# Optimization experiments

Measured on AMD Instinct MI355X. Metric: run time of the kernel, lower is better.

Reference implementation:

```python
import math
import jax, jax.numpy as jnp
import numpy as np

S = 2048
D_MOD = 1024
D_K = 64
D_V = 64
H = 16
MASKED = True


def setup_inputs() -> dict:
    key = jax.random.key(0)
    ks = jax.random.split(key, 11)
    sc_in = 1.0 / math.sqrt(D_MOD)
    sc_o = 1.0 / math.sqrt(H * D_V)
    return {
        "Q_input": jax.random.normal(ks[0], (S, D_MOD), jnp.float32),
        "K_input": jax.random.normal(ks[1], (S, D_MOD), jnp.float32),
        "V_input": jax.random.normal(ks[2], (S, D_MOD), jnp.float32),
        # stacked per-head Linear params (torch Linear: y = x @ W.T + b)
        "WQw": jax.random.uniform(ks[3], (H, D_K, D_MOD), jnp.float32, -sc_in, sc_in),
        "WQb": jax.random.uniform(ks[4], (H, D_K), jnp.float32, -sc_in, sc_in),
        "WKw": jax.random.uniform(ks[5], (H, D_K, D_MOD), jnp.float32, -sc_in, sc_in),
        "WKb": jax.random.uniform(ks[6], (H, D_K), jnp.float32, -sc_in, sc_in),
        "WVw": jax.random.uniform(ks[7], (H, D_V, D_MOD), jnp.float32, -sc_in, sc_in),
        "WVb": jax.random.uniform(ks[8], (H, D_V), jnp.float32, -sc_in, sc_in),
        "WOw": jax.random.uniform(ks[9], (D_MOD, H * D_V), jnp.float32, -sc_o, sc_o),
        "WOb": jax.random.uniform(ks[10], (D_MOD,), jnp.float32, -sc_o, sc_o),
    }


def reference(Q_input, K_input, V_input, WQw, WQb, WKw, WKb, WVw, WVb, WOw, WOb):
    # per-head projections, batched over heads: [H, S, d]
    q = jnp.einsum("sd,hkd->hsk", Q_input, WQw) + WQb[:, None, :]
    k = jnp.einsum("sd,hkd->hsk", K_input, WKw) + WKb[:, None, :]
    v = jnp.einsum("sd,hvd->hsv", V_input, WVw) + WVb[:, None, :]
    # raw scores [H, S, T]
    qk = jnp.einsum("hsk,htk->hst", q, k)
    if MASKED:
        qk = jnp.tril(qk)  # torch.tril: zero (not -inf) upper triangle
    # torch log_softmax(dim=0) on each [S, T] matrix -> axis 1 of [H, S, T]
    scores = jax.nn.log_softmax(qk / math.sqrt(D_K), axis=1)
    attn = jnp.einsum("hst,htv->hsv", scores, v)  # [H, S, d_v]
    # torch.cat(head_attns, dim=1) -> [S, H*d_v], head-major feature order
    Z = jnp.transpose(attn, (1, 0, 2)).reshape(S, H * D_V)
    return Z @ WOw.T + WOb
```

## Files before the change

### kernel.cpp

```cpp
#include <hip/hip_runtime.h>
#include <math.h>
#include <stdint.h>

#define S 2048
#define DMOD 1024
#define H 16

typedef unsigned short ushort_t;
typedef short bf16x8 __attribute__((ext_vector_type(8)));
typedef float f32x4 __attribute__((ext_vector_type(4)));

#define SW(r) ((((r) & 7)) ^ ((((r) >> 3) & 3) << 1))

__device__ __forceinline__ ushort_t f2b(float f) {
    union { float f; unsigned u; } x; x.f = f;
    return (ushort_t)((x.u + 0x7FFFu + ((x.u >> 16) & 1u)) >> 16);
}
__device__ __forceinline__ float b2f(ushort_t b) {
    union { unsigned u; float f; } x; x.u = ((unsigned)b) << 16;
    return x.f;
}
__device__ __forceinline__ void gld16(const ushort_t* g, ushort_t* l) {
    __builtin_amdgcn_global_load_lds(
        (const __attribute__((address_space(1))) unsigned int*)g,
        (__attribute__((address_space(3))) unsigned int*)l, 16, 0, 0);
}

__global__ __launch_bounds__(256) void init_all(
    float* __restrict__ attn_raw, float* __restrict__ out,
    float* __restrict__ sumexp, float* __restrict__ corr)
{
    const int b = blockIdx.x;
    const float4 z4 = {0.f, 0.f, 0.f, 0.f};
    if (b < 2048) {
        *(float4*)(attn_raw + ((size_t)b * 256 + threadIdx.x) * 4) = z4;
    } else if (b < 4096) {
        *(float4*)(out + ((size_t)(b - 2048) * 256 + threadIdx.x) * 4) = z4;
    } else if (b < 4128) {
        int e = ((b - 4096) * 256 + threadIdx.x) * 4;
        float4 v = {(float)(e & 2047), (float)((e + 1) & 2047),
                    (float)((e + 2) & 2047), (float)((e + 3) & 2047)};
        *(float4*)(sumexp + e) = v;
    } else {
        *(float4*)(corr + threadIdx.x * 4) = z4;
    }
}

__global__ __launch_bounds__(256) void convert_all(
    const float* q, const float* k, const float* v,
    const float* wq, const float* wk, const float* wv, const float* wo,
    ushort_t* qo, ushort_t* ko, ushort_t* vo,
    ushort_t* wqo, ushort_t* wko, ushort_t* wvo, ushort_t* woo)
{
    const int seg = blockIdx.y;
    const float* src; ushort_t* dst; size_t off = 0;
    const size_t M1 = (size_t)1 << 20;
    if (seg < 2)       { src = q;  dst = qo;  off = (size_t)seg * M1; }
    else if (seg < 4)  { src = k;  dst = ko;  off = (size_t)(seg - 2) * M1; }
    else if (seg < 6)  { src = v;  dst = vo;  off = (size_t)(seg - 4) * M1; }
    else if (seg == 6) { src = wq; dst = wqo; }
    else if (seg == 7) { src = wk; dst = wko; }
    else if (seg == 8) { src = wv; dst = wvo; }
    else               { src = wo; dst = woo; }
    size_t i = off + ((size_t)blockIdx.x * 256 + threadIdx.x) * 4;
    float4 f = *(const float4*)(src + i);
    union { uint2 u2; ushort_t us[4]; } o;
    o.us[0] = f2b(f.x); o.us[1] = f2b(f.y); o.us[2] = f2b(f.z); o.us[3] = f2b(f.w);
    *(uint2*)(dst + i) = o.u2;
}

__global__ __launch_bounds__(256) void gemm_qkv(
    const ushort_t* __restrict__ A0, const ushort_t* __restrict__ A1,
    const ushort_t* __restrict__ A2, const ushort_t* __restrict__ Wqkv,
    const float* __restrict__ b0, const float* __restrict__ b1,
    const float* __restrict__ b2,
    ushort_t* __restrict__ qbb, ushort_t* __restrict__ kbb,
    ushort_t* __restrict__ vt)
{
    __shared__ ushort_t As[128 * 64];
    __shared__ ushort_t Bs[64 * 64];
    const int tid = threadIdx.x;
    const int lane = tid & 63, wid = tid >> 6;
    const int quad = lane >> 4, l15 = lane & 15;
    const int wr = wid >> 1, wc = wid & 1;
    const int m0 = blockIdx.y * 128;
    const int n0 = blockIdx.x * 64;
    const int seg = n0 >> 10;
    const int nloc = n0 & 1023;
    const ushort_t* A = seg == 0 ? A0 : (seg == 1 ? A1 : A2);
    const float* bias = seg == 0 ? b0 : (seg == 1 ? b1 : b2);

    const f32x4 fz = {0.f, 0.f, 0.f, 0.f};
    f32x4 acc[4][2];
#pragma unroll
    for (int i = 0; i < 4; ++i) { acc[i][0] = fz; acc[i][1] = fz; }

    for (int k0 = 0; k0 < DMOD; k0 += 64) {
        __syncthreads();
#pragma unroll
        for (int i = 0; i < 4; ++i) {
            int c = i * 256 + tid, row = c >> 3, kcl = c & 7;
            gld16(A + (size_t)(m0 + row) * DMOD + k0 + (kcl ^ SW(row)) * 8, &As[c * 8]);
        }
#pragma unroll
        for (int i = 0; i < 2; ++i) {
            int c = i * 256 + tid, row = c >> 3, kcl = c & 7;
            gld16(Wqkv + (size_t)(n0 + row) * DMOD + k0 + (kcl ^ SW(row)) * 8, &Bs[c * 8]);
        }
        __syncthreads();
#pragma unroll
        for (int kc = 0; kc < 2; ++kc) {
            bf16x8 af[4], bfr[2];
#pragma unroll
            for (int mi = 0; mi < 4; ++mi) {
                int row = wr * 64 + mi * 16 + l15;
                af[mi] = *(const bf16x8*)&As[row * 64 + ((kc * 4 + quad) ^ SW(row)) * 8];
            }
#pragma unroll
            for (int ni = 0; ni < 2; ++ni) {
                int row = wc * 32 + ni * 16 + l15;
                bfr[ni] = *(const bf16x8*)&Bs[row * 64 + ((kc * 4 + quad) ^ SW(row)) * 8];
            }
#pragma unroll
            for (int mi = 0; mi < 4; ++mi)
#pragma unroll
                for (int ni = 0; ni < 2; ++ni)
                    acc[mi][ni] = __builtin_amdgcn_mfma_f32_16x16x32_bf16(
                        af[mi], bfr[ni], acc[mi][ni], 0, 0, 0);
        }
    }

    if (seg < 2) {
        ushort_t* C = seg == 0 ? qbb : kbb;
#pragma unroll
        for (int mi = 0; mi < 4; ++mi)
#pragma unroll
            for (int ni = 0; ni < 2; ++ni) {
                int gn = nloc + wc * 32 + ni * 16 + l15;
                float bv = bias[gn];
#pragma unroll
                for (int r = 0; r < 4; ++r) {
                    int gm = m0 + wr * 64 + mi * 16 + quad * 4 + r;
                    C[(size_t)gm * DMOD + gn] = f2b(acc[mi][ni][r] + bv);
                }
            }
    } else {
#pragma unroll
        for (int mi = 0; mi < 4; ++mi)
#pragma unroll
            for (int ni = 0; ni < 2; ++ni) {
                int gn = nloc + wc * 32 + ni * 16 + l15;
                float bv = bias[gn];
                int gmb = m0 + wr * 64 + mi * 16 + quad * 4;
                union { uint2 u2; ushort_t us[4]; } o;
#pragma unroll
                for (int r = 0; r < 4; ++r) o.us[r] = f2b(acc[mi][ni][r] + bv);
                *(uint2*)&vt[(size_t)gn * S + gmb] = o.u2;
            }
    }
}

__global__ __launch_bounds__(512, 4) void attn_mfma(
    const ushort_t* __restrict__ qb, const ushort_t* __restrict__ kb,
    const ushort_t* __restrict__ vt, float* __restrict__ attn_raw,
    float* __restrict__ sumexp)
{
    __shared__ ushort_t Qs[128 * 64];
    __shared__ ushort_t Ks[2][4096];
    __shared__ ushort_t Vs[2][4096];
    __shared__ ushort_t Ps[128 * 64];
    __shared__ float    sacc[1024];

    const int h = blockIdx.y;
    const int bx = blockIdx.x;
    const int si = 15 - (bx >> 1);
    const int z = bx & 1;
    const int half = si + 1;
    const int tbeg = z ? half : 0;
    const int tend = z ? 2 * si + 2 : half;
    const int s0 = si * 128;

    const int tid = threadIdx.x;
    const int lane = tid & 63, w = tid >> 6;
    const int quad = lane >> 4, l15 = lane & 15;
    const int sband = s0 + w * 16;

    const ushort_t* qh = qb + h * 64;
    const ushort_t* kh = kb + h * 64;
    const ushort_t* vh = vt + (size_t)(h * 64) * S;

#pragma unroll
    for (int i = 0; i < 2; ++i) {
        int c = i * 512 + tid, row = c >> 3, kcl = c & 7;
        gld16(qh + (size_t)(s0 + row) * DMOD + (kcl ^ SW(row)) * 8, &Qs[c * 8]);
    }
    {
        int t0 = tbeg * 64;
        int row = tid >> 3, kcl = tid & 7;
        gld16(kh + (size_t)(t0 + row) * DMOD + (kcl ^ SW(row)) * 8, &Ks[0][tid * 8]);
        gld16(vh + (size_t)row * S + t0 + (kcl ^ SW(row)) * 8, &Vs[0][tid * 8]);
    }
    for (int i = tid; i < 1024; i += 512) sacc[i] = 0.f;
    __syncthreads();

    bf16x8 aq[2];
    {
        int rq = w * 16 + l15;
#pragma unroll
        for (int kc = 0; kc < 2; ++kc)
            aq[kc] = *(const bf16x8*)&Qs[rq * 64 + ((kc * 4 + quad) ^ SW(rq)) * 8];
    }

    const f32x4 fz = {0.f, 0.f, 0.f, 0.f};
    f32x4 oacc[4];
#pragma unroll
    for (int ni = 0; ni < 4; ++ni) oacc[ni] = fz;

    for (int it = tbeg; it < tend; ++it) {
        const int p = (it - tbeg) & 1;
        const int t0 = it * 64;
        if (it + 1 < tend) {
            int t1 = t0 + 64;
            int row = tid >> 3, kcl = tid & 7;
            gld16(kh + (size_t)(t1 + row) * DMOD + (kcl ^ SW(row)) * 8, &Ks[1 - p][tid * 8]);
            gld16(vh + (size_t)row * S + t1 + (kcl ^ SW(row)) * 8, &Vs[1 - p][tid * 8]);
        }

        if (t0 < sband + 16) {
            f32x4 xf[4];
#pragma unroll
            for (int ti = 0; ti < 4; ++ti) xf[ti] = fz;
#pragma unroll
            for (int kc = 0; kc < 2; ++kc) {
#pragma unroll
                for (int ti = 0; ti < 4; ++ti) {
                    int rk = ti * 16 + l15;
                    bf16x8 bk = *(const bf16x8*)&Ks[p][rk * 64 + ((kc * 4 + quad) ^ SW(rk)) * 8];
                    xf[ti] = __builtin_amdgcn_mfma_f32_16x16x32_bf16(aq[kc], bk, xf[ti], 0, 0, 0);
                }
            }

            const bool clean = (t0 + 63 <= sband);
            const int s_q = sband + quad * 4;
#pragma unroll
            for (int ti = 0; ti < 4; ++ti) {
                int t_g = t0 + ti * 16 + l15;
                float es = 0.f;
#pragma unroll
                for (int r = 0; r < 4; ++r) {
                    float xv = xf[ti][r] * 0.125f;
                    bool live = clean || (s_q + r >= t_g);
                    xv = live ? xv : 0.f;
                    es += live ? __expf(xv) : 0.f;
                    xf[ti][r] = xv;
                }
                es += __shfl_xor(es, 16, 64);
                es += __shfl_xor(es, 32, 64);
                if (quad == 0) atomicAdd(&sacc[t0 - tbeg * 64 + ti * 16 + l15], es);
#pragma unroll
                for (int r = 0; r < 4; ++r) {
                    int sl = w * 16 + quad * 4 + r;
                    int tc = ti * 16 + l15;
                    Ps[sl * 64 + ((tc >> 3) ^ SW(sl)) * 8 + (tc & 7)] = f2b(xf[ti][r]);
                }
            }

#pragma unroll
            for (int kc = 0; kc < 2; ++kc) {
                int rp = w * 16 + l15;
                bf16x8 ap = *(const bf16x8*)&Ps[rp * 64 + ((kc * 4 + quad) ^ SW(rp)) * 8];
#pragma unroll
                for (int ni = 0; ni < 4; ++ni) {
                    int rv = ni * 16 + l15;
                    bf16x8 bv = *(const bf16x8*)&Vs[p][rv * 64 + ((kc * 4 + quad) ^ SW(rv)) * 8];
                    oacc[ni] = __builtin_amdgcn_mfma_f32_16x16x32_bf16(ap, bv, oacc[ni], 0, 0, 0);
                }
            }
        }
        __syncthreads();
    }

    {
        int nv = (tend - tbeg) * 64;
        for (int i = tid; i < nv; i += 512)
            atomicAdd(&sumexp[h * S + tbeg * 64 + i], sacc[i]);
    }
#pragma unroll
    for (int ni = 0; ni < 4; ++ni)
#pragma unroll
        for (int r = 0; r < 4; ++r) {
            int s_g = s0 + w * 16 + quad * 4 + r;
            atomicAdd(&attn_raw[(size_t)s_g * DMOD + h * 64 + ni * 16 + l15],
                      oacc[ni][r]);
        }
}

__global__ __launch_bounds__(256) void corr_kernel(
    const float* __restrict__ sumexp, const ushort_t* __restrict__ vt,
    float* __restrict__ corr)
{
    const int w = threadIdx.x >> 6, lane = threadIdx.x & 63;
    const int r = blockIdx.x * 4 + w;
    const int h = r >> 6;
    float acc = 0.f;
#pragma unroll
    for (int i = 0; i < 4; ++i) {
        int t = i * 512 + lane * 8;
        bf16x8 vv = *(const bf16x8*)&vt[(size_t)r * S + t];
        float4 s0 = *(const float4*)&sumexp[h * S + t];
        float4 s1 = *(const float4*)&sumexp[h * S + t + 4];
        acc += logf(s0.x) * b2f((ushort_t)vv[0]) + logf(s0.y) * b2f((ushort_t)vv[1])
             + logf(s0.z) * b2f((ushort_t)vv[2]) + logf(s0.w) * b2f((ushort_t)vv[3])
             + logf(s1.x) * b2f((ushort_t)vv[4]) + logf(s1.y) * b2f((ushort_t)vv[5])
             + logf(s1.z) * b2f((ushort_t)vv[6]) + logf(s1.w) * b2f((ushort_t)vv[7]);
    }
#pragma unroll
    for (int d = 1; d < 64; d <<= 1) acc += __shfl_xor(acc, d, 64);
    if (lane == 0) corr[r] = acc;
}

__global__ __launch_bounds__(256) void convert_Z(
    const float* __restrict__ attn_raw, const float* __restrict__ corr,
    ushort_t* __restrict__ Zb)
{
    size_t i = ((size_t)blockIdx.x * 256 + threadIdx.x) * 4;
    float4 f = *(const float4*)(attn_raw + i);
    int c = (int)(i & (DMOD - 1));
    union { uint2 u2; ushort_t us[4]; } o;
    o.us[0] = f2b(f.x - corr[c]);
    o.us[1] = f2b(f.y - corr[c + 1]);
    o.us[2] = f2b(f.z - corr[c + 2]);
    o.us[3] = f2b(f.w - corr[c + 3]);
    *(uint2*)(Zb + i) = o.u2;
}

__global__ __launch_bounds__(256) void gemm_out(
    const ushort_t* __restrict__ A, const ushort_t* __restrict__ W,
    const float* __restrict__ bias, float* __restrict__ C)
{
    __shared__ ushort_t As[128 * 64];
    __shared__ ushort_t Bs[64 * 64];
    const int tid = threadIdx.x;
    const int lane = tid & 63, wid = tid >> 6;
    const int quad = lane >> 4, l15 = lane & 15;
    const int wr = wid >> 1, wc = wid & 1;
    const int m0 = blockIdx.y * 128, n0 = blockIdx.x * 64;
    const int kbeg = blockIdx.z * 512, kend = kbeg + 512;

    const f32x4 fz = {0.f, 0.f, 0.f, 0.f};
    f32x4 acc[4][2];
#pragma unroll
    for (int i = 0; i < 4; ++i) { acc[i][0] = fz; acc[i][1] = fz; }

    for (int k0 = kbeg; k0 < kend; k0 += 64) {
        __syncthreads();
#pragma unroll
        for (int i = 0; i < 4; ++i) {
            int c = i * 256 + tid, row = c >> 3, kcl = c & 7;
            gld16(A + (size_t)(m0 + row) * DMOD + k0 + (kcl ^ SW(row)) * 8, &As[c * 8]);
        }
#pragma unroll
        for (int i = 0; i < 2; ++i) {
            int c = i * 256 + tid, row = c >> 3, kcl = c & 7;
            gld16(W + (size_t)(n0 + row) * DMOD + k0 + (kcl ^ SW(row)) * 8, &Bs[c * 8]);
        }
        __syncthreads();
#pragma unroll
        for (int kc = 0; kc < 2; ++kc) {
            bf16x8 af[4], bfr[2];
#pragma unroll
            for (int mi = 0; mi < 4; ++mi) {
                int row = wr * 64 + mi * 16 + l15;
                af[mi] = *(const bf16x8*)&As[row * 64 + ((kc * 4 + quad) ^ SW(row)) * 8];
            }
#pragma unroll
            for (int ni = 0; ni < 2; ++ni) {
                int row = wc * 32 + ni * 16 + l15;
                bfr[ni] = *(const bf16x8*)&Bs[row * 64 + ((kc * 4 + quad) ^ SW(row)) * 8];
            }
#pragma unroll
            for (int mi = 0; mi < 4; ++mi)
#pragma unroll
                for (int ni = 0; ni < 2; ++ni)
                    acc[mi][ni] = __builtin_amdgcn_mfma_f32_16x16x32_bf16(
                        af[mi], bfr[ni], acc[mi][ni], 0, 0, 0);
        }
    }
#pragma unroll
    for (int mi = 0; mi < 4; ++mi)
#pragma unroll
        for (int ni = 0; ni < 2; ++ni) {
            int gn = n0 + wc * 32 + ni * 16 + l15;
            float bv = (kbeg == 0) ? bias[gn] : 0.f;
#pragma unroll
            for (int r = 0; r < 4; ++r) {
                int gm = m0 + wr * 64 + mi * 16 + quad * 4 + r;
                atomicAdd(&C[(size_t)gm * DMOD + gn], acc[mi][ni][r] + bv);
            }
        }
}

extern "C" void kernel_launch(void* const* d_in, const int* in_sizes, int n_in,
                              void* d_out, int out_size, void* d_ws, size_t ws_size,
                              hipStream_t stream) {
    const float* Qin = (const float*)d_in[0];
    const float* Kin = (const float*)d_in[1];
    const float* Vin = (const float*)d_in[2];
    const float* WQw = (const float*)d_in[3];
    const float* WQb = (const float*)d_in[4];
    const float* WKw = (const float*)d_in[5];
    const float* WKb = (const float*)d_in[6];
    const float* WVw = (const float*)d_in[7];
    const float* WVb = (const float*)d_in[8];
    const float* WOw = (const float*)d_in[9];
    const float* WOb = (const float*)d_in[10];

    float* ws = (float*)d_ws;
    const size_t M1 = (size_t)1 << 20;
    ushort_t* qbb  = (ushort_t*)(ws);
    ushort_t* kbb  = (ushort_t*)(ws + M1);
    ushort_t* vt   = (ushort_t*)(ws + 2 * M1);
    ushort_t* wqkv = (ushort_t*)(ws + 3 * M1);
    ushort_t* wob  = (ushort_t*)(ws + 4 * M1 + M1 / 2);
    ushort_t* Qbin = (ushort_t*)(ws + 5 * M1);
    ushort_t* Kbin = (ushort_t*)(ws + 6 * M1);
    ushort_t* Vbin = (ushort_t*)(ws + 7 * M1);
    float* attn_raw = ws + 6 * M1;
    ushort_t* Zb    = (ushort_t*)(ws + 5 * M1);
    float* sumexp   = ws + 8 * M1;
    float* corr     = ws + 8 * M1 + H * S;

    init_all<<<4129, 256, 0, stream>>>(attn_raw, (float*)d_out, sumexp, corr);

    convert_all<<<dim3(1024, 10), 256, 0, stream>>>(
        Qin, Kin, Vin, WQw, WKw, WVw, WOw,
        Qbin, Kbin, Vbin,
        wqkv, wqkv + (size_t)1024 * 1024, wqkv + (size_t)2 * 1024 * 1024, wob);

    gemm_qkv<<<dim3(48, 16), 256, 0, stream>>>(
        Qbin, Kbin, Vbin, wqkv, WQb, WKb, WVb, qbb, kbb, vt);

    attn_mfma<<<dim3(32, H), 512, 0, stream>>>(qbb, kbb, vt, attn_raw, sumexp);

    corr_kernel<<<256, 256, 0, stream>>>(sumexp, vt, corr);
    convert_Z<<<2048, 256, 0, stream>>>(attn_raw, corr, Zb);

    gemm_out<<<dim3(16, 16, 2), 256, 0, stream>>>(Zb, wob, WOb, (float*)d_out);
}
```

Measured before the change: 203.8 us.

## Split causal attention key range four ways and share Q/P shared-memory buffer

Each 128-row query block's key range is now split across four blocks instead of two, using balanced chunk sizes. This doubles the attention grid to improve load balance and SM fill. The Q and P shared-memory tiles are merged into one buffer and the exp-sum scratch is halved, to allow a higher occupancy target in launch bounds. Warps with no unmasked key tile skip their atomic adds to attn_raw. The finer split still adds more global atomic traffic on the partial outputs and sums.

```diff
diff --git a/kernel.cpp b/kernel.cpp
--- a/kernel.cpp
+++ b/kernel.cpp
@@ -160,24 +160,26 @@
     }
 }
 
-__global__ __launch_bounds__(512, 4) void attn_mfma(
+__global__ __launch_bounds__(512, 6) void attn_mfma(
     const ushort_t* __restrict__ qb, const ushort_t* __restrict__ kb,
     const ushort_t* __restrict__ vt, float* __restrict__ attn_raw,
     float* __restrict__ sumexp)
 {
-    __shared__ ushort_t Qs[128 * 64];
+    __shared__ ushort_t QPs[128 * 64];
     __shared__ ushort_t Ks[2][4096];
     __shared__ ushort_t Vs[2][4096];
-    __shared__ ushort_t Ps[128 * 64];
-    __shared__ float    sacc[1024];
+    __shared__ float    sacc[512];
 
     const int h = blockIdx.y;
     const int bx = blockIdx.x;
-    const int si = 15 - (bx >> 1);
-    const int z = bx & 1;
-    const int half = si + 1;
-    const int tbeg = z ? half : 0;
-    const int tend = z ? 2 * si + 2 : half;
+    const int si = 15 - (bx >> 2);
+    const int zq = bx & 3;
+    const int nt = 2 * si + 2;
+    const int base = nt >> 2, rem = nt & 3;
+    const int tbeg = zq * base + (zq < rem ? zq : rem);
+    const int cnt  = base + (zq < rem ? 1 : 0);
+    const int tend = tbeg + cnt;
+    if (cnt == 0) return;
     const int s0 = si * 128;
 
     const int tid = threadIdx.x;
@@ -192,7 +194,7 @@
 #pragma unroll
     for (int i = 0; i < 2; ++i) {
         int c = i * 512 + tid, row = c >> 3, kcl = c & 7;
-        gld16(qh + (size_t)(s0 + row) * DMOD + (kcl ^ SW(row)) * 8, &Qs[c * 8]);
+        gld16(qh + (size_t)(s0 + row) * DMOD + (kcl ^ SW(row)) * 8, &QPs[c * 8]);
     }
     {
         int t0 = tbeg * 64;
@@ -200,7 +202,7 @@
         gld16(kh + (size_t)(t0 + row) * DMOD + (kcl ^ SW(row)) * 8, &Ks[0][tid * 8]);
         gld16(vh + (size_t)row * S + t0 + (kcl ^ SW(row)) * 8, &Vs[0][tid * 8]);
     }
-    for (int i = tid; i < 1024; i += 512) sacc[i] = 0.f;
+    if (tid < 512) sacc[tid] = 0.f;
     __syncthreads();
 
     bf16x8 aq[2];
@@ -208,13 +210,14 @@
         int rq = w * 16 + l15;
 #pragma unroll
         for (int kc = 0; kc < 2; ++kc)
-            aq[kc] = *(const bf16x8*)&Qs[rq * 64 + ((kc * 4 + quad) ^ SW(rq)) * 8];
+            aq[kc] = *(const bf16x8*)&QPs[rq * 64 + ((kc * 4 + quad) ^ SW(rq)) * 8];
     }
 
     const f32x4 fz = {0.f, 0.f, 0.f, 0.f};
     f32x4 oacc[4];
 #pragma unroll
     for (int ni = 0; ni < 4; ++ni) oacc[ni] = fz;
+    bool any_live = false;
 
     for (int it = tbeg; it < tend; ++it) {
         const int p = (it - tbeg) & 1;
@@ -227,6 +230,7 @@
         }
 
         if (t0 < sband + 16) {
+            any_live = true;
             f32x4 xf[4];
 #pragma unroll
             for (int ti = 0; ti < 4; ++ti) xf[ti] = fz;
@@ -256,19 +260,19 @@
                 }
                 es += __shfl_xor(es, 16, 64);
                 es += __shfl_xor(es, 32, 64);
-                if (quad == 0) atomicAdd(&sacc[t0 - tbeg * 64 + ti * 16 + l15], es);
+                if (quad == 0) atomicAdd(&sacc[(it - tbeg) * 64 + ti * 16 + l15], es);
 #pragma unroll
                 for (int r = 0; r < 4; ++r) {
                     int sl = w * 16 + quad * 4 + r;
                     int tc = ti * 16 + l15;
-                    Ps[sl * 64 + ((tc >> 3) ^ SW(sl)) * 8 + (tc & 7)] = f2b(xf[ti][r]);
+                    QPs[sl * 64 + ((tc >> 3) ^ SW(sl)) * 8 + (tc & 7)] = f2b(xf[ti][r]);
                 }
             }
 
 #pragma unroll
             for (int kc = 0; kc < 2; ++kc) {
                 int rp = w * 16 + l15;
-                bf16x8 ap = *(const bf16x8*)&Ps[rp * 64 + ((kc * 4 + quad) ^ SW(rp)) * 8];
+                bf16x8 ap = *(const bf16x8*)&QPs[rp * 64 + ((kc * 4 + quad) ^ SW(rp)) * 8];
 #pragma unroll
                 for (int ni = 0; ni < 4; ++ni) {
                     int rv = ni * 16 + l15;
@@ -281,18 +285,20 @@
     }
 
     {
-        int nv = (tend - tbeg) * 64;
+        int nv = cnt * 64;
         for (int i = tid; i < nv; i += 512)
             atomicAdd(&sumexp[h * S + tbeg * 64 + i], sacc[i]);
     }
-#pragma unroll
-    for (int ni = 0; ni < 4; ++ni)
-#pragma unroll
-        for (int r = 0; r < 4; ++r) {
-            int s_g = s0 + w * 16 + quad * 4 + r;
-            atomicAdd(&attn_raw[(size_t)s_g * DMOD + h * 64 + ni * 16 + l15],
-                      oacc[ni][r]);
-        }
+    if (any_live) {
+#pragma unroll
+        for (int ni = 0; ni < 4; ++ni)
+#pragma unroll
+            for (int r = 0; r < 4; ++r) {
+                int s_g = s0 + w * 16 + quad * 4 + r;
+                atomicAdd(&attn_raw[(size_t)s_g * DMOD + h * 64 + ni * 16 + l15],
+                          oacc[ni][r]);
+            }
+    }
 }
 
 __global__ __launch_bounds__(256) void corr_kernel(
@@ -440,7 +446,7 @@
     gemm_qkv<<<dim3(48, 16), 256, 0, stream>>>(
         Qbin, Kbin, Vbin, wqkv, WQb, WKb, WVb, qbb, kbb, vt);
 
-    attn_mfma<<<dim3(32, H), 512, 0, stream>>>(qbb, kbb, vt, attn_raw, sumexp);
+    attn_mfma<<<dim3(64, H), 512, 0, stream>>>(qbb, kbb, vt, attn_raw, sumexp);
 
     corr_kernel<<<256, 256, 0, stream>>>(sumexp, vt, corr);
     convert_Z<<<2048, 256, 0, stream>>>(attn_raw, corr, Zb);
```

Result: slower. 231.9 us (+13.8%).
